# Kernel tuning notes

Measured on AMD Instinct MI355X. Metric: run time of the kernel, lower is better.

## Reference

```python
import jax, jax.numpy as jnp
import numpy as np

INPUT = 28
HID = 64
OUT = 10


def setup_inputs() -> dict:
    key = jax.random.key(0)
    ks = jax.random.split(key, 8)
    s_ih = 1.0 / np.sqrt(HID)
    x = jax.random.normal(ks[0], (16384, 28, INPUT), dtype=jnp.float32)
    # PyTorch LSTM params: gate order (i, f, g, o), each block of size HID
    W_ih = jax.random.uniform(ks[1], (4 * HID, INPUT), jnp.float32, -s_ih, s_ih)
    W_hh = jax.random.uniform(ks[2], (4 * HID, HID), jnp.float32, -s_ih, s_ih)
    b_ih = jax.random.uniform(ks[3], (4 * HID,), jnp.float32, -s_ih, s_ih)
    b_hh = jax.random.uniform(ks[4], (4 * HID,), jnp.float32, -s_ih, s_ih)
    s_fc = 1.0 / np.sqrt(HID)
    W_fc = jax.random.uniform(ks[5], (OUT, HID), jnp.float32, -s_fc, s_fc)
    b_fc = jax.random.uniform(ks[6], (OUT,), jnp.float32, -s_fc, s_fc)
    return {"x": x, "W_ih": W_ih, "W_hh": W_hh, "b_ih": b_ih, "b_hh": b_hh,
            "W_fc": W_fc, "b_fc": b_fc}


def reference(x, W_ih, W_hh, b_ih, b_hh, W_fc, b_fc):
    B = x.shape[0]
    # Precompute input projections for all timesteps in one big GEMM: [T, B, 4H]
    x_proj = jnp.einsum('bti,gi->tbg', x, W_ih) + (b_ih + b_hh)

    def step(carry, xp_t):
        h, c = carry
        gates = xp_t + h @ W_hh.T  # [B, 4H]
        i, f, g, o = jnp.split(gates, 4, axis=-1)
        i = jax.nn.sigmoid(i)
        f = jax.nn.sigmoid(f)
        g = jnp.tanh(g)
        o = jax.nn.sigmoid(o)
        c = f * c + i * g
        h = o * jnp.tanh(c)
        return (h, c), None

    h0 = jnp.zeros((B, HID), dtype=x.dtype)
    c0 = jnp.zeros((B, HID), dtype=x.dtype)
    (h_last, _), _ = jax.lax.scan(step, (h0, c0), x_proj)
    # fc on the last timestep's hidden state (== output[:, -1, :])
    return h_last @ W_fc.T + b_fc
```

## Files before the change

kernel.cpp:

```cpp
#include <hip/hip_runtime.h>
#include <hip/hip_bf16.h>


namespace {
constexpr int B_TOT   = 16384;
constexpr int T_STEPS = 28;
constexpr int IN_DIM  = 28;
constexpr int HID     = 64;
constexpr int OUT_DIM = 10;
constexpr int ROWS    = 16;
constexpr int THREADS = 512;
constexpr int KP      = 104;
constexpr int XROW    = T_STEPS * IN_DIM;
constexpr int NFRAG   = 16 * 3;
constexpr int WS_ELEMS = NFRAG * 64 * 8;
}

typedef __attribute__((ext_vector_type(8))) short short8v;
typedef __attribute__((ext_vector_type(4))) short short4v;
typedef __attribute__((ext_vector_type(4))) float float4v;

__device__ __forceinline__ short f2bf_cold(float f) {
  union { float f; unsigned u; } v; v.f = f;
  unsigned r = v.u + 0x7FFFu + ((v.u >> 16) & 1u);
  return (short)(r >> 16);
}
__device__ __forceinline__ float bf2f(short s) {
  union { unsigned u; float f; } v; v.u = ((unsigned)(unsigned short)s) << 16;
  return v.f;
}
__device__ __forceinline__ unsigned pk2(float a, float b) {
  __hip_bfloat162 h = __float22bfloat162_rn(float2{a, b});
  union { __hip_bfloat162 h; unsigned u; } cv; cv.h = h; return cv.u;
}

__global__ void lstm_prep(const float* __restrict__ W_ih,
                          const float* __restrict__ W_hh,
                          const float* __restrict__ b_ih,
                          const float* __restrict__ b_hh,
                          unsigned short* __restrict__ ws) {
  int idx = blockIdx.x * blockDim.x + threadIdx.x;
  if (idx >= WS_ELEMS) return;
  int j  = idx & 7;
  int l  = (idx >> 3) & 63;
  int fk = idx >> 9;
  int kc = fk % 3;
  int mt = fk / 3;
  int m  = 16 * mt + (l & 15);
  int unit = m >> 2, type = m & 3;
  int g  = type * 64 + unit;
  int k  = kc * 32 + (l >> 4) * 8 + j;
  float v = 0.0f;
  if (k < IN_DIM)        v = W_ih[g * IN_DIM + k];
  else if (k == IN_DIM)  v = b_ih[g] + b_hh[g];
  else if (k >= 32) {
    int c = k - 32;
    int u = 8 * (c >> 3) + 4 * (c & 1) + ((c >> 1) & 3);
    v = W_hh[g * HID + u];
  }
  v *= (type == 2) ? -2.8853900817779268f : -1.4426950408889634f;
  ws[idx] = (unsigned short)f2bf_cold(v);
}

__global__ __attribute__((amdgpu_flat_work_group_size(THREADS, THREADS),
                          amdgpu_waves_per_eu(8, 8)))
void lstm_mfma8(const float* __restrict__ x,
                const unsigned short* __restrict__ wfrag,
                const float* __restrict__ W_fc,
                const float* __restrict__ b_fc, float* __restrict__ out) {
  __shared__ short hs[2][ROWS][KP];

  const int tid  = threadIdx.x;
  const int lane = tid & 63;
  const int w    = tid >> 6;
  const int l15  = lane & 15;
  const int q    = lane >> 4;
  const int b0   = blockIdx.x * ROWS;

  short8v a[2][3];
#pragma unroll
  for (int i = 0; i < 2; ++i)
#pragma unroll
    for (int kc = 0; kc < 3; ++kc)
      a[i][kc] = *(const short8v*)&wfrag[((((2 * w + i) * 3) + kc) * 64 + lane) * 8];

  for (int idx = tid; idx < 2 * ROWS * KP; idx += THREADS) (&hs[0][0][0])[idx] = 0;
  __syncthreads();
  if (tid < 2 * ROWS) hs[tid >> 4][tid & 15][IN_DIM] = (short)0x3F80;

  const bool stager = (lane < 14);
  const int  s  = w * 14 + lane;
  const int  sr = s / 7;
  const int  sc = s - 7 * sr;
  const float* xptr = x + (size_t)(b0 + sr) * XROW + sc * 4;

  float4 xfly = {0.f, 0.f, 0.f, 0.f};
  if (stager) {
    float4 x0 = *(const float4*)xptr;
    short4v sv;
    unsigned plo = pk2(x0.x, x0.y), phi = pk2(x0.z, x0.w);
    sv[0] = (short)(plo & 0xFFFF); sv[1] = (short)(plo >> 16);
    sv[2] = (short)(phi & 0xFFFF); sv[3] = (short)(phi >> 16);
    *(short4v*)&hs[0][sr][sc * 4] = sv;
    xfly = *(const float4*)(xptr + 1 * IN_DIM);
  }
  __syncthreads();

  float c_state[2] = {0.f, 0.f};

  for (int t = 0; t < T_STEPS; ++t) {
    const int cur = t & 1, nxt = cur ^ 1;

    short8v bf0 = *(const short8v*)&hs[cur][l15][q * 8];
    short8v bf1 = *(const short8v*)&hs[cur][l15][32 + q * 8];
    short8v bf2 = *(const short8v*)&hs[cur][l15][64 + q * 8];

    if (stager) {
      if (t + 1 < T_STEPS) {
        short4v sv;
        unsigned plo = pk2(xfly.x, xfly.y), phi = pk2(xfly.z, xfly.w);
        sv[0] = (short)(plo & 0xFFFF); sv[1] = (short)(plo >> 16);
        sv[2] = (short)(phi & 0xFFFF); sv[3] = (short)(phi >> 16);
        *(short4v*)&hs[nxt][sr][sc * 4] = sv;
      }
      if (t + 2 < T_STEPS)
        xfly = *(const float4*)(xptr + (t + 2) * IN_DIM);
    }

    const float4v zero4 = {0.f, 0.f, 0.f, 0.f};
    float4v acc[2];
#pragma unroll
    for (int i = 0; i < 2; ++i)
      acc[i] = __builtin_amdgcn_mfma_f32_16x16x32_bf16(a[i][0], bf0, zero4, 0, 0, 0);
#pragma unroll
    for (int i = 0; i < 2; ++i)
      acc[i] = __builtin_amdgcn_mfma_f32_16x16x32_bf16(a[i][1], bf1, acc[i], 0, 0, 0);
#pragma unroll
    for (int i = 0; i < 2; ++i)
      acc[i] = __builtin_amdgcn_mfma_f32_16x16x32_bf16(a[i][2], bf2, acc[i], 0, 0, 0);

    float hv[2];
#pragma unroll
    for (int i = 0; i < 2; ++i) {
      float4v g4 = acc[i];
      float Ei = __builtin_amdgcn_exp2f(g4[0]);
      float Ef = __builtin_amdgcn_exp2f(g4[1]);
      float Eg = __builtin_amdgcn_exp2f(g4[2]);
      float Eo = __builtin_amdgcn_exp2f(g4[3]);
      float di = 1.0f + Ei, df = 1.0f + Ef;
      float r1 = __builtin_amdgcn_rcpf(di * df);
      float iv = r1 * df;
      float fv = r1 * di;
      float gv = fmaf(2.0f, __builtin_amdgcn_rcpf(1.0f + Eg), -1.0f);
      float cn = fmaf(fv, c_state[i], iv * gv);
      c_state[i] = cn;
      float ct = fminf(fmaxf(cn, -15.0f), 15.0f);
      float Ec = __builtin_amdgcn_exp2f(-2.8853900817779268f * ct);
      float dn = 1.0f + Eo, dc = 1.0f + Ec;
      float r2 = __builtin_amdgcn_rcpf(dn * dc);
      float ov = r2 * dc;
      float tc = fmaf(2.0f * r2, dn, -1.0f);
      hv[i] = ov * tc;
    }
    unsigned p01 = pk2(hv[0], hv[1]);
    *(unsigned*)&hs[nxt][l15][32 + 8 * w + 2 * q] = p01;

    __syncthreads();
  }

  if (tid < ROWS * OUT_DIM) {
    const int r = tid / OUT_DIM;
    const int o = tid - r * OUT_DIM;
    float sacc = b_fc[o];
#pragma unroll
    for (int c = 0; c < HID; ++c) {
      int u = 8 * (c >> 3) + 4 * (c & 1) + ((c >> 1) & 3);
      sacc += bf2f(hs[0][r][32 + c]) * W_fc[o * HID + u];
    }
    out[(b0 + r) * OUT_DIM + o] = sacc;
  }
}

extern "C" void kernel_launch(void* const* d_in, const int* in_sizes, int n_in,
                              void* d_out, int out_size, void* d_ws, size_t ws_size,
                              hipStream_t stream) {
  const float* x    = (const float*)d_in[0];
  const float* W_ih = (const float*)d_in[1];
  const float* W_hh = (const float*)d_in[2];
  const float* b_ih = (const float*)d_in[3];
  const float* b_hh = (const float*)d_in[4];
  const float* W_fc = (const float*)d_in[5];
  const float* b_fc = (const float*)d_in[6];
  float* out = (float*)d_out;
  unsigned short* ws = (unsigned short*)d_ws;

  lstm_prep<<<(WS_ELEMS + 255) / 256, 256, 0, stream>>>(W_ih, W_hh, b_ih, b_hh, ws);

  dim3 grid(B_TOT / ROWS);
  dim3 block(THREADS);
  lstm_mfma8<<<grid, block, 0, stream>>>(x, ws, W_fc, b_fc, out);
}
```

Baseline: 133.1 us.

## Process two 16-row batch groups per block to interleave independent recurrences

Each block now handles two independent 16-row batch groups, with separate LDS hidden-state buffers and cell states. Each wave issues MFMAs and gate math for both groups between barriers, which gives the scheduler independent work to hide MFMA and transcendental latency. The number of barriers per row is halved and the register-held weight fragments are reused across both groups. In exchange the grid is halved, register use roughly doubles for accumulators, and the occupancy hint drops from 8 to 4 waves per EU.

```diff
diff --git a/kernel.cpp b/kernel.cpp
--- a/kernel.cpp
+++ b/kernel.cpp
@@ -9,6 +9,7 @@
 constexpr int HID     = 64;
 constexpr int OUT_DIM = 10;
 constexpr int ROWS    = 16;
+constexpr int GROUPS  = 2;
 constexpr int THREADS = 512;
 constexpr int KP      = 104;
 constexpr int XROW    = T_STEPS * IN_DIM;
@@ -63,19 +64,19 @@
 }
 
 __global__ __attribute__((amdgpu_flat_work_group_size(THREADS, THREADS),
-                          amdgpu_waves_per_eu(8, 8)))
+                          amdgpu_waves_per_eu(4, 4)))
 void lstm_mfma8(const float* __restrict__ x,
                 const unsigned short* __restrict__ wfrag,
                 const float* __restrict__ W_fc,
                 const float* __restrict__ b_fc, float* __restrict__ out) {
-  __shared__ short hs[2][ROWS][KP];
+  __shared__ short hs[GROUPS][2][ROWS][KP];
 
   const int tid  = threadIdx.x;
   const int lane = tid & 63;
   const int w    = tid >> 6;
   const int l15  = lane & 15;
   const int q    = lane >> 4;
-  const int b0   = blockIdx.x * ROWS;
+  const int b0   = blockIdx.x * (ROWS * GROUPS);
 
   short8v a[2][3];
 #pragma unroll
@@ -84,15 +85,18 @@
     for (int kc = 0; kc < 3; ++kc)
       a[i][kc] = *(const short8v*)&wfrag[((((2 * w + i) * 3) + kc) * 64 + lane) * 8];
 
-  for (int idx = tid; idx < 2 * ROWS * KP; idx += THREADS) (&hs[0][0][0])[idx] = 0;
+  for (int idx = tid; idx < GROUPS * 2 * ROWS * KP; idx += THREADS)
+    (&hs[0][0][0][0])[idx] = 0;
   __syncthreads();
-  if (tid < 2 * ROWS) hs[tid >> 4][tid & 15][IN_DIM] = (short)0x3F80;
-
-  const bool stager = (lane < 14);
-  const int  s  = w * 14 + lane;
+  if (tid < GROUPS * 2 * ROWS)
+    hs[tid >> 5][(tid >> 4) & 1][tid & 15][IN_DIM] = (short)0x3F80;
+
+  const bool stager = (lane < 28);
+  const int  sg = (lane >= 14) ? 1 : 0;
+  const int  s  = w * 14 + (lane - 14 * sg);
   const int  sr = s / 7;
   const int  sc = s - 7 * sr;
-  const float* xptr = x + (size_t)(b0 + sr) * XROW + sc * 4;
+  const float* xptr = x + (size_t)(b0 + sg * ROWS + sr) * XROW + sc * 4;
 
   float4 xfly = {0.f, 0.f, 0.f, 0.f};
   if (stager) {
@@ -101,19 +105,23 @@
     unsigned plo = pk2(x0.x, x0.y), phi = pk2(x0.z, x0.w);
     sv[0] = (short)(plo & 0xFFFF); sv[1] = (short)(plo >> 16);
     sv[2] = (short)(phi & 0xFFFF); sv[3] = (short)(phi >> 16);
-    *(short4v*)&hs[0][sr][sc * 4] = sv;
+    *(short4v*)&hs[sg][0][sr][sc * 4] = sv;
     xfly = *(const float4*)(xptr + 1 * IN_DIM);
   }
   __syncthreads();
 
-  float c_state[2] = {0.f, 0.f};
+  float c_state[GROUPS][2] = {{0.f, 0.f}, {0.f, 0.f}};
 
   for (int t = 0; t < T_STEPS; ++t) {
     const int cur = t & 1, nxt = cur ^ 1;
 
-    short8v bf0 = *(const short8v*)&hs[cur][l15][q * 8];
-    short8v bf1 = *(const short8v*)&hs[cur][l15][32 + q * 8];
-    short8v bf2 = *(const short8v*)&hs[cur][l15][64 + q * 8];
+    short8v bf[GROUPS][3];
+#pragma unroll
+    for (int gg = 0; gg < GROUPS; ++gg) {
+      bf[gg][0] = *(const short8v*)&hs[gg][cur][l15][q * 8];
+      bf[gg][1] = *(const short8v*)&hs[gg][cur][l15][32 + q * 8];
+      bf[gg][2] = *(const short8v*)&hs[gg][cur][l15][64 + q * 8];
+    }
 
     if (stager) {
       if (t + 1 < T_STEPS) {
@@ -121,63 +129,70 @@
         unsigned plo = pk2(xfly.x, xfly.y), phi = pk2(xfly.z, xfly.w);
         sv[0] = (short)(plo & 0xFFFF); sv[1] = (short)(plo >> 16);
         sv[2] = (short)(phi & 0xFFFF); sv[3] = (short)(phi >> 16);
-        *(short4v*)&hs[nxt][sr][sc * 4] = sv;
+        *(short4v*)&hs[sg][nxt][sr][sc * 4] = sv;
       }
       if (t + 2 < T_STEPS)
         xfly = *(const float4*)(xptr + (t + 2) * IN_DIM);
     }
 
     const float4v zero4 = {0.f, 0.f, 0.f, 0.f};
-    float4v acc[2];
-#pragma unroll
-    for (int i = 0; i < 2; ++i)
-      acc[i] = __builtin_amdgcn_mfma_f32_16x16x32_bf16(a[i][0], bf0, zero4, 0, 0, 0);
-#pragma unroll
-    for (int i = 0; i < 2; ++i)
-      acc[i] = __builtin_amdgcn_mfma_f32_16x16x32_bf16(a[i][1], bf1, acc[i], 0, 0, 0);
-#pragma unroll
-    for (int i = 0; i < 2; ++i)
-      acc[i] = __builtin_amdgcn_mfma_f32_16x16x32_bf16(a[i][2], bf2, acc[i], 0, 0, 0);
-
-    float hv[2];
-#pragma unroll
-    for (int i = 0; i < 2; ++i) {
-      float4v g4 = acc[i];
-      float Ei = __builtin_amdgcn_exp2f(g4[0]);
-      float Ef = __builtin_amdgcn_exp2f(g4[1]);
-      float Eg = __builtin_amdgcn_exp2f(g4[2]);
-      float Eo = __builtin_amdgcn_exp2f(g4[3]);
-      float di = 1.0f + Ei, df = 1.0f + Ef;
-      float r1 = __builtin_amdgcn_rcpf(di * df);
-      float iv = r1 * df;
-      float fv = r1 * di;
-      float gv = fmaf(2.0f, __builtin_amdgcn_rcpf(1.0f + Eg), -1.0f);
-      float cn = fmaf(fv, c_state[i], iv * gv);
-      c_state[i] = cn;
-      float ct = fminf(fmaxf(cn, -15.0f), 15.0f);
-      float Ec = __builtin_amdgcn_exp2f(-2.8853900817779268f * ct);
-      float dn = 1.0f + Eo, dc = 1.0f + Ec;
-      float r2 = __builtin_amdgcn_rcpf(dn * dc);
-      float ov = r2 * dc;
-      float tc = fmaf(2.0f * r2, dn, -1.0f);
-      hv[i] = ov * tc;
-    }
-    unsigned p01 = pk2(hv[0], hv[1]);
-    *(unsigned*)&hs[nxt][l15][32 + 8 * w + 2 * q] = p01;
+    float4v acc[GROUPS][2];
+#pragma unroll
+    for (int gg = 0; gg < GROUPS; ++gg) {
+#pragma unroll
+      for (int i = 0; i < 2; ++i)
+        acc[gg][i] = __builtin_amdgcn_mfma_f32_16x16x32_bf16(a[i][0], bf[gg][0], zero4, 0, 0, 0);
+#pragma unroll
+      for (int i = 0; i < 2; ++i)
+        acc[gg][i] = __builtin_amdgcn_mfma_f32_16x16x32_bf16(a[i][1], bf[gg][1], acc[gg][i], 0, 0, 0);
+#pragma unroll
+      for (int i = 0; i < 2; ++i)
+        acc[gg][i] = __builtin_amdgcn_mfma_f32_16x16x32_bf16(a[i][2], bf[gg][2], acc[gg][i], 0, 0, 0);
+    }
+
+#pragma unroll
+    for (int gg = 0; gg < GROUPS; ++gg) {
+      float hv[2];
+#pragma unroll
+      for (int i = 0; i < 2; ++i) {
+        float4v g4 = acc[gg][i];
+        float Ei = __builtin_amdgcn_exp2f(g4[0]);
+        float Ef = __builtin_amdgcn_exp2f(g4[1]);
+        float Eg = __builtin_amdgcn_exp2f(g4[2]);
+        float Eo = __builtin_amdgcn_exp2f(g4[3]);
+        float di = 1.0f + Ei, df = 1.0f + Ef;
+        float r1 = __builtin_amdgcn_rcpf(di * df);
+        float iv = r1 * df;
+        float fv = r1 * di;
+        float gv = fmaf(2.0f, __builtin_amdgcn_rcpf(1.0f + Eg), -1.0f);
+        float cn = fmaf(fv, c_state[gg][i], iv * gv);
+        c_state[gg][i] = cn;
+        float ct = fminf(fmaxf(cn, -15.0f), 15.0f);
+        float Ec = __builtin_amdgcn_exp2f(-2.8853900817779268f * ct);
+        float dn = 1.0f + Eo, dc = 1.0f + Ec;
+        float r2 = __builtin_amdgcn_rcpf(dn * dc);
+        float ov = r2 * dc;
+        float tc = fmaf(2.0f * r2, dn, -1.0f);
+        hv[i] = ov * tc;
+      }
+      unsigned p01 = pk2(hv[0], hv[1]);
+      *(unsigned*)&hs[gg][nxt][l15][32 + 8 * w + 2 * q] = p01;
+    }
 
     __syncthreads();
   }
 
-  if (tid < ROWS * OUT_DIM) {
+  if (tid < GROUPS * ROWS * OUT_DIM) {
     const int r = tid / OUT_DIM;
     const int o = tid - r * OUT_DIM;
+    const int gg = r >> 4, rr = r & 15;
     float sacc = b_fc[o];
 #pragma unroll
     for (int c = 0; c < HID; ++c) {
       int u = 8 * (c >> 3) + 4 * (c & 1) + ((c >> 1) & 3);
-      sacc += bf2f(hs[0][r][32 + c]) * W_fc[o * HID + u];
-    }
-    out[(b0 + r) * OUT_DIM + o] = sacc;
+      sacc += bf2f(hs[gg][0][rr][32 + c]) * W_fc[o * HID + u];
+    }
+    out[(b0 + gg * ROWS + rr) * OUT_DIM + o] = sacc;
   }
 }
 
@@ -196,7 +211,7 @@
 
   lstm_prep<<<(WS_ELEMS + 255) / 256, 256, 0, stream>>>(W_ih, W_hh, b_ih, b_hh, ws);
 
-  dim3 grid(B_TOT / ROWS);
+  dim3 grid(B_TOT / (ROWS * GROUPS));
   dim3 block(THREADS);
   lstm_mfma8<<<grid, block, 0, stream>>>(x, ws, W_fc, b_fc, out);
 }
```

Result: no change. 134.6 us (+1.1%).

## Run each 16-row LSTM tile in a single wave holding all gate weights

Applied to the files above, without the earlier changes.

The block shrinks from eight waves to one wave of 64 threads, and each wave now keeps all 16 M-tiles of the gate weight fragments in registers. This removes the per-timestep __syncthreads and replaces it with an LDS waitcnt fence. The hidden-unit permutation is changed so each lane writes its 16 h values as two contiguous 16-byte stores, and the FC epilogue is remapped to 64 lanes. The trade-off is many more VGPRs per wave (48 weight fragments plus 16 accumulators) at one wave per EU, so it relies on having enough blocks to hide MFMA and transcendental latency, and there may be register spills.

```diff
diff --git a/kernel.cpp b/kernel.cpp
--- a/kernel.cpp
+++ b/kernel.cpp
@@ -9,7 +9,7 @@
 constexpr int HID     = 64;
 constexpr int OUT_DIM = 10;
 constexpr int ROWS    = 16;
-constexpr int THREADS = 512;
+constexpr int THREADS = 64;
 constexpr int KP      = 104;
 constexpr int XROW    = T_STEPS * IN_DIM;
 constexpr int NFRAG   = 16 * 3;
@@ -19,6 +19,11 @@
 typedef __attribute__((ext_vector_type(8))) short short8v;
 typedef __attribute__((ext_vector_type(4))) short short4v;
 typedef __attribute__((ext_vector_type(4))) float float4v;
+
+__device__ __forceinline__ void lds_fence() {
+  asm volatile("s_waitcnt lgkmcnt(0)" ::: "memory");
+  __builtin_amdgcn_sched_barrier(0);
+}
 
 __device__ __forceinline__ short f2bf_cold(float f) {
   union { float f; unsigned u; } v; v.f = f;
@@ -55,7 +60,7 @@
   else if (k == IN_DIM)  v = b_ih[g] + b_hh[g];
   else if (k >= 32) {
     int c = k - 32;
-    int u = 8 * (c >> 3) + 4 * (c & 1) + ((c >> 1) & 3);
+    int u = 4 * (c & 15) + (c >> 4);
     v = W_hh[g * HID + u];
   }
   v *= (type == 2) ? -2.8853900817779268f : -1.4426950408889634f;
@@ -63,86 +68,109 @@
 }
 
 __global__ __attribute__((amdgpu_flat_work_group_size(THREADS, THREADS),
-                          amdgpu_waves_per_eu(8, 8)))
-void lstm_mfma8(const float* __restrict__ x,
-                const unsigned short* __restrict__ wfrag,
-                const float* __restrict__ W_fc,
-                const float* __restrict__ b_fc, float* __restrict__ out) {
-  __shared__ short hs[2][ROWS][KP];
-
-  const int tid  = threadIdx.x;
-  const int lane = tid & 63;
-  const int w    = tid >> 6;
+                          amdgpu_waves_per_eu(1, 1)))
+void lstm_wave(const float* __restrict__ x,
+               const unsigned short* __restrict__ wfrag,
+               const float* __restrict__ W_fc,
+               const float* __restrict__ b_fc, float* __restrict__ out) {
+  __shared__ __align__(16) short hs[2][ROWS][KP];
+
+  const int lane = threadIdx.x & 63;
   const int l15  = lane & 15;
   const int q    = lane >> 4;
   const int b0   = blockIdx.x * ROWS;
 
-  short8v a[2][3];
-#pragma unroll
-  for (int i = 0; i < 2; ++i)
+  short8v a[16][3];
+#pragma unroll
+  for (int mt = 0; mt < 16; ++mt)
 #pragma unroll
     for (int kc = 0; kc < 3; ++kc)
-      a[i][kc] = *(const short8v*)&wfrag[((((2 * w + i) * 3) + kc) * 64 + lane) * 8];
-
-  for (int idx = tid; idx < 2 * ROWS * KP; idx += THREADS) (&hs[0][0][0])[idx] = 0;
-  __syncthreads();
-  if (tid < 2 * ROWS) hs[tid >> 4][tid & 15][IN_DIM] = (short)0x3F80;
-
-  const bool stager = (lane < 14);
-  const int  s  = w * 14 + lane;
-  const int  sr = s / 7;
-  const int  sc = s - 7 * sr;
-  const float* xptr = x + (size_t)(b0 + sr) * XROW + sc * 4;
-
-  float4 xfly = {0.f, 0.f, 0.f, 0.f};
-  if (stager) {
-    float4 x0 = *(const float4*)xptr;
+      a[mt][kc] = *(const short8v*)&wfrag[(((mt * 3) + kc) * 64 + lane) * 8];
+
+  {
+    short4v z4 = {0, 0, 0, 0};
+#pragma unroll
+    for (int k2 = 0; k2 < 13; ++k2)
+      ((short4v*)&hs[0][0][0])[lane + 64 * k2] = z4;
+  }
+  lds_fence();
+  if (lane < 2 * ROWS)
+    hs[lane >> 4][lane & 15][IN_DIM] = (short)0x3F80;
+
+  const int  s0  = lane;
+  const int  s1  = lane + 64;
+  const bool st1 = (s1 < 112);
+  const int  sr0 = s0 / 7, sc0 = s0 - 7 * sr0;
+  const int  sr1 = st1 ? (s1 / 7) : 0, sc1 = st1 ? (s1 - 7 * (s1 / 7)) : 0;
+  const float* xp0 = x + (size_t)(b0 + sr0) * XROW + sc0 * 4;
+  const float* xp1 = x + (size_t)(b0 + sr1) * XROW + sc1 * 4;
+
+  float4 fly0, fly1 = {0.f, 0.f, 0.f, 0.f};
+  {
+    float4 x0 = *(const float4*)xp0;
     short4v sv;
     unsigned plo = pk2(x0.x, x0.y), phi = pk2(x0.z, x0.w);
     sv[0] = (short)(plo & 0xFFFF); sv[1] = (short)(plo >> 16);
     sv[2] = (short)(phi & 0xFFFF); sv[3] = (short)(phi >> 16);
-    *(short4v*)&hs[0][sr][sc * 4] = sv;
-    xfly = *(const float4*)(xptr + 1 * IN_DIM);
-  }
-  __syncthreads();
-
-  float c_state[2] = {0.f, 0.f};
+    *(short4v*)&hs[0][sr0][sc0 * 4] = sv;
+    if (st1) {
+      float4 x1 = *(const float4*)xp1;
+      unsigned qlo = pk2(x1.x, x1.y), qhi = pk2(x1.z, x1.w);
+      sv[0] = (short)(qlo & 0xFFFF); sv[1] = (short)(qlo >> 16);
+      sv[2] = (short)(qhi & 0xFFFF); sv[3] = (short)(qhi >> 16);
+      *(short4v*)&hs[0][sr1][sc1 * 4] = sv;
+    }
+    fly0 = *(const float4*)(xp0 + 1 * IN_DIM);
+    if (st1) fly1 = *(const float4*)(xp1 + 1 * IN_DIM);
+  }
+
+  float c_state[16];
+#pragma unroll
+  for (int mt = 0; mt < 16; ++mt) c_state[mt] = 0.f;
 
   for (int t = 0; t < T_STEPS; ++t) {
     const int cur = t & 1, nxt = cur ^ 1;
+
+    lds_fence();
 
     short8v bf0 = *(const short8v*)&hs[cur][l15][q * 8];
     short8v bf1 = *(const short8v*)&hs[cur][l15][32 + q * 8];
     short8v bf2 = *(const short8v*)&hs[cur][l15][64 + q * 8];
 
-    if (stager) {
-      if (t + 1 < T_STEPS) {
-        short4v sv;
-        unsigned plo = pk2(xfly.x, xfly.y), phi = pk2(xfly.z, xfly.w);
-        sv[0] = (short)(plo & 0xFFFF); sv[1] = (short)(plo >> 16);
-        sv[2] = (short)(phi & 0xFFFF); sv[3] = (short)(phi >> 16);
-        *(short4v*)&hs[nxt][sr][sc * 4] = sv;
+    if (t + 1 < T_STEPS) {
+      short4v sv;
+      unsigned plo = pk2(fly0.x, fly0.y), phi = pk2(fly0.z, fly0.w);
+      sv[0] = (short)(plo & 0xFFFF); sv[1] = (short)(plo >> 16);
+      sv[2] = (short)(phi & 0xFFFF); sv[3] = (short)(phi >> 16);
+      *(short4v*)&hs[nxt][sr0][sc0 * 4] = sv;
+      if (st1) {
+        unsigned qlo = pk2(fly1.x, fly1.y), qhi = pk2(fly1.z, fly1.w);
+        sv[0] = (short)(qlo & 0xFFFF); sv[1] = (short)(qlo >> 16);
+        sv[2] = (short)(qhi & 0xFFFF); sv[3] = (short)(qhi >> 16);
+        *(short4v*)&hs[nxt][sr1][sc1 * 4] = sv;
       }
-      if (t + 2 < T_STEPS)
-        xfly = *(const float4*)(xptr + (t + 2) * IN_DIM);
+      if (t + 2 < T_STEPS) {
+        fly0 = *(const float4*)(xp0 + (t + 2) * IN_DIM);
+        if (st1) fly1 = *(const float4*)(xp1 + (t + 2) * IN_DIM);
+      }
     }
 
     const float4v zero4 = {0.f, 0.f, 0.f, 0.f};
-    float4v acc[2];
-#pragma unroll
-    for (int i = 0; i < 2; ++i)
-      acc[i] = __builtin_amdgcn_mfma_f32_16x16x32_bf16(a[i][0], bf0, zero4, 0, 0, 0);
-#pragma unroll
-    for (int i = 0; i < 2; ++i)
-      acc[i] = __builtin_amdgcn_mfma_f32_16x16x32_bf16(a[i][1], bf1, acc[i], 0, 0, 0);
-#pragma unroll
-    for (int i = 0; i < 2; ++i)
-      acc[i] = __builtin_amdgcn_mfma_f32_16x16x32_bf16(a[i][2], bf2, acc[i], 0, 0, 0);
-
-    float hv[2];
-#pragma unroll
-    for (int i = 0; i < 2; ++i) {
-      float4v g4 = acc[i];
+    float4v acc[16];
+#pragma unroll
+    for (int mt = 0; mt < 16; ++mt)
+      acc[mt] = __builtin_amdgcn_mfma_f32_16x16x32_bf16(a[mt][0], bf0, zero4, 0, 0, 0);
+#pragma unroll
+    for (int mt = 0; mt < 16; ++mt)
+      acc[mt] = __builtin_amdgcn_mfma_f32_16x16x32_bf16(a[mt][1], bf1, acc[mt], 0, 0, 0);
+#pragma unroll
+    for (int mt = 0; mt < 16; ++mt)
+      acc[mt] = __builtin_amdgcn_mfma_f32_16x16x32_bf16(a[mt][2], bf2, acc[mt], 0, 0, 0);
+
+    float hv[16];
+#pragma unroll
+    for (int mt = 0; mt < 16; ++mt) {
+      float4v g4 = acc[mt];
       float Ei = __builtin_amdgcn_exp2f(g4[0]);
       float Ef = __builtin_amdgcn_exp2f(g4[1]);
       float Eg = __builtin_amdgcn_exp2f(g4[2]);
@@ -152,32 +180,46 @@
       float iv = r1 * df;
       float fv = r1 * di;
       float gv = fmaf(2.0f, __builtin_amdgcn_rcpf(1.0f + Eg), -1.0f);
-      float cn = fmaf(fv, c_state[i], iv * gv);
-      c_state[i] = cn;
+      float cn = fmaf(fv, c_state[mt], iv * gv);
+      c_state[mt] = cn;
       float ct = fminf(fmaxf(cn, -15.0f), 15.0f);
       float Ec = __builtin_amdgcn_exp2f(-2.8853900817779268f * ct);
       float dn = 1.0f + Eo, dc = 1.0f + Ec;
       float r2 = __builtin_amdgcn_rcpf(dn * dc);
       float ov = r2 * dc;
       float tc = fmaf(2.0f * r2, dn, -1.0f);
-      hv[i] = ov * tc;
-    }
-    unsigned p01 = pk2(hv[0], hv[1]);
-    *(unsigned*)&hs[nxt][l15][32 + 8 * w + 2 * q] = p01;
-
-    __syncthreads();
-  }
-
-  if (tid < ROWS * OUT_DIM) {
-    const int r = tid / OUT_DIM;
-    const int o = tid - r * OUT_DIM;
-    float sacc = b_fc[o];
+      hv[mt] = ov * tc;
+    }
+
+    union { unsigned u[4]; short8v s; } uh0, uh1;
+#pragma unroll
+    for (int p = 0; p < 4; ++p) uh0.u[p] = pk2(hv[2 * p], hv[2 * p + 1]);
+#pragma unroll
+    for (int p = 0; p < 4; ++p) uh1.u[p] = pk2(hv[8 + 2 * p], hv[9 + 2 * p]);
+    *(short8v*)&hs[nxt][l15][32 + 16 * q]     = uh0.s;
+    *(short8v*)&hs[nxt][l15][32 + 16 * q + 8] = uh1.s;
+  }
+
+  lds_fence();
+
+  {
+    const int er = lane >> 2;
+    const int eo = lane & 3;
+    float s0a = b_fc[eo];
+    float s1a = b_fc[eo + 4];
+    float s2a = (eo < 2) ? b_fc[eo + 8] : 0.f;
 #pragma unroll
     for (int c = 0; c < HID; ++c) {
-      int u = 8 * (c >> 3) + 4 * (c & 1) + ((c >> 1) & 3);
-      sacc += bf2f(hs[0][r][32 + c]) * W_fc[o * HID + u];
-    }
-    out[(b0 + r) * OUT_DIM + o] = sacc;
+      float hb = bf2f(hs[0][er][32 + c]);
+      int u = 4 * (c & 15) + (c >> 4);
+      s0a = fmaf(hb, W_fc[eo * HID + u], s0a);
+      s1a = fmaf(hb, W_fc[(eo + 4) * HID + u], s1a);
+      if (eo < 2) s2a = fmaf(hb, W_fc[(eo + 8) * HID + u], s2a);
+    }
+    float* orow = out + (size_t)(b0 + er) * OUT_DIM;
+    orow[eo]     = s0a;
+    orow[eo + 4] = s1a;
+    if (eo < 2) orow[eo + 8] = s2a;
   }
 }
 
@@ -198,5 +240,5 @@
 
   dim3 grid(B_TOT / ROWS);
   dim3 block(THREADS);
-  lstm_mfma8<<<grid, block, 0, stream>>>(x, ws, W_fc, b_fc, out);
-}
+  lstm_wave<<<grid, block, 0, stream>>>(x, ws, W_fc, b_fc, out);
+}
```

Result: slower. 138.3 us (+3.9%).

## Use 2 waves per block with 8 gate tiles each and AGPR-pinned weights

Applied to the files above, without the earlier changes.

Shrinks each 16-row block from 8 waves to 2 waves, so each wave computes 8 MFMA gate tiles instead of 2. Weight fragments are pinned in accumulator registers through an inline asm constraint. The hidden-state permutation is changed so each lane writes 8 contiguous bf16 values with one 16-byte store. The aim is fewer waves per barrier and wider LDS stores, at the cost of far more registers per wave and lower occupancy (waves_per_eu 2). Per-wave MFMA serial work per step rises, which could lengthen the recurrence critical path.

```diff
diff --git a/kernel.cpp b/kernel.cpp
--- a/kernel.cpp
+++ b/kernel.cpp
@@ -9,7 +9,7 @@
 constexpr int HID     = 64;
 constexpr int OUT_DIM = 10;
 constexpr int ROWS    = 16;
-constexpr int THREADS = 512;
+constexpr int THREADS = 128;
 constexpr int KP      = 104;
 constexpr int XROW    = T_STEPS * IN_DIM;
 constexpr int NFRAG   = 16 * 3;
@@ -55,7 +55,7 @@
   else if (k == IN_DIM)  v = b_ih[g] + b_hh[g];
   else if (k >= 32) {
     int c = k - 32;
-    int u = 8 * (c >> 3) + 4 * (c & 1) + ((c >> 1) & 3);
+    int u = 4 * (c & 15) + (c >> 4);
     v = W_hh[g * HID + u];
   }
   v *= (type == 2) ? -2.8853900817779268f : -1.4426950408889634f;
@@ -63,12 +63,12 @@
 }
 
 __global__ __attribute__((amdgpu_flat_work_group_size(THREADS, THREADS),
-                          amdgpu_waves_per_eu(8, 8)))
-void lstm_mfma8(const float* __restrict__ x,
-                const unsigned short* __restrict__ wfrag,
-                const float* __restrict__ W_fc,
-                const float* __restrict__ b_fc, float* __restrict__ out) {
-  __shared__ short hs[2][ROWS][KP];
+                          amdgpu_waves_per_eu(2, 2)))
+void lstm_wave(const float* __restrict__ x,
+               const unsigned short* __restrict__ wfrag,
+               const float* __restrict__ W_fc,
+               const float* __restrict__ b_fc, float* __restrict__ out) {
+  __shared__ __align__(16) short hs[2][ROWS][KP];
 
   const int tid  = threadIdx.x;
   const int lane = tid & 63;
@@ -77,22 +77,30 @@
   const int q    = lane >> 4;
   const int b0   = blockIdx.x * ROWS;
 
-  short8v a[2][3];
-#pragma unroll
-  for (int i = 0; i < 2; ++i)
+  short8v a[8][3];
+#pragma unroll
+  for (int i = 0; i < 8; ++i)
 #pragma unroll
     for (int kc = 0; kc < 3; ++kc)
-      a[i][kc] = *(const short8v*)&wfrag[((((2 * w + i) * 3) + kc) * 64 + lane) * 8];
-
-  for (int idx = tid; idx < 2 * ROWS * KP; idx += THREADS) (&hs[0][0][0])[idx] = 0;
+      a[i][kc] = *(const short8v*)&wfrag[((((8 * w + i) * 3) + kc) * 64 + lane) * 8];
+#pragma unroll
+  for (int i = 0; i < 8; ++i)
+#pragma unroll
+    for (int kc = 0; kc < 3; ++kc)
+      asm volatile("" : "+a"(a[i][kc]));
+
+  {
+    short4v z4 = {0, 0, 0, 0};
+    for (int idx = tid; idx < 2 * ROWS * KP / 4; idx += THREADS)
+      ((short4v*)&hs[0][0][0])[idx] = z4;
+  }
   __syncthreads();
-  if (tid < 2 * ROWS) hs[tid >> 4][tid & 15][IN_DIM] = (short)0x3F80;
-
-  const bool stager = (lane < 14);
-  const int  s  = w * 14 + lane;
-  const int  sr = s / 7;
-  const int  sc = s - 7 * sr;
-  const float* xptr = x + (size_t)(b0 + sr) * XROW + sc * 4;
+  if (tid < 2 * ROWS)
+    hs[tid >> 4][tid & 15][IN_DIM] = (short)0x3F80;
+
+  const bool stager = (tid < 112);
+  const int  sr = tid / 7, sc = tid - 7 * (tid / 7);
+  const float* xptr = x + (size_t)(b0 + (stager ? sr : 0)) * XROW + sc * 4;
 
   float4 xfly = {0.f, 0.f, 0.f, 0.f};
   if (stager) {
@@ -106,7 +114,9 @@
   }
   __syncthreads();
 
-  float c_state[2] = {0.f, 0.f};
+  float c_state[8];
+#pragma unroll
+  for (int i = 0; i < 8; ++i) c_state[i] = 0.f;
 
   for (int t = 0; t < T_STEPS; ++t) {
     const int cur = t & 1, nxt = cur ^ 1;
@@ -128,20 +138,20 @@
     }
 
     const float4v zero4 = {0.f, 0.f, 0.f, 0.f};
-    float4v acc[2];
-#pragma unroll
-    for (int i = 0; i < 2; ++i)
+    float4v acc[8];
+#pragma unroll
+    for (int i = 0; i < 8; ++i)
       acc[i] = __builtin_amdgcn_mfma_f32_16x16x32_bf16(a[i][0], bf0, zero4, 0, 0, 0);
 #pragma unroll
-    for (int i = 0; i < 2; ++i)
+    for (int i = 0; i < 8; ++i)
       acc[i] = __builtin_amdgcn_mfma_f32_16x16x32_bf16(a[i][1], bf1, acc[i], 0, 0, 0);
 #pragma unroll
-    for (int i = 0; i < 2; ++i)
+    for (int i = 0; i < 8; ++i)
       acc[i] = __builtin_amdgcn_mfma_f32_16x16x32_bf16(a[i][2], bf2, acc[i], 0, 0, 0);
 
-    float hv[2];
-#pragma unroll
-    for (int i = 0; i < 2; ++i) {
+    float hv[8];
+#pragma unroll
+    for (int i = 0; i < 8; ++i) {
       float4v g4 = acc[i];
       float Ei = __builtin_amdgcn_exp2f(g4[0]);
       float Ef = __builtin_amdgcn_exp2f(g4[1]);
@@ -162,22 +172,30 @@
       float tc = fmaf(2.0f * r2, dn, -1.0f);
       hv[i] = ov * tc;
     }
-    unsigned p01 = pk2(hv[0], hv[1]);
-    *(unsigned*)&hs[nxt][l15][32 + 8 * w + 2 * q] = p01;
+
+    union { unsigned u[4]; short8v s; } uh;
+#pragma unroll
+    for (int p = 0; p < 4; ++p) uh.u[p] = pk2(hv[2 * p], hv[2 * p + 1]);
+    *(short8v*)&hs[nxt][l15][32 + 16 * q + 8 * w] = uh.s;
 
     __syncthreads();
   }
 
-  if (tid < ROWS * OUT_DIM) {
-    const int r = tid / OUT_DIM;
-    const int o = tid - r * OUT_DIM;
-    float sacc = b_fc[o];
+  {
+    const int er = tid >> 3;
+    const int eo = tid & 7;
+    float s0a = b_fc[eo];
+    float s2a = (eo < 2) ? b_fc[eo + 8] : 0.f;
 #pragma unroll
     for (int c = 0; c < HID; ++c) {
-      int u = 8 * (c >> 3) + 4 * (c & 1) + ((c >> 1) & 3);
-      sacc += bf2f(hs[0][r][32 + c]) * W_fc[o * HID + u];
+      float hb = bf2f(hs[0][er][32 + c]);
+      int u = 4 * (c & 15) + (c >> 4);
+      s0a = fmaf(hb, W_fc[eo * HID + u], s0a);
+      if (eo < 2) s2a = fmaf(hb, W_fc[(eo + 8) * HID + u], s2a);
     }
-    out[(b0 + r) * OUT_DIM + o] = sacc;
+    float* orow = out + (size_t)(b0 + er) * OUT_DIM;
+    orow[eo] = s0a;
+    if (eo < 2) orow[eo + 8] = s2a;
   }
 }
 
@@ -198,5 +216,5 @@
 
   dim3 grid(B_TOT / ROWS);
   dim3 block(THREADS);
-  lstm_mfma8<<<grid, block, 0, stream>>>(x, ws, W_fc, b_fc, out);
-}
+  lstm_wave<<<grid, block, 0, stream>>>(x, ws, W_fc, b_fc, out);
+}
```

Result: slower. 138.1 us (+3.8%).
